# Kernel optimization log

Measured on AMD Instinct MI355X. Metric: run time of the kernel, lower is better.

Reference implementation:

```python
import jax, jax.numpy as jnp
import numpy as np

D_MODEL, D_STATE, D_CONV, EXPAND, HEADDIM, NGROUPS, CHUNK = 1024, 64, 4, 2, 64, 1, 64
D_INNER = EXPAND * D_MODEL          # 2048
NHEADS = D_INNER // HEADDIM         # 32
CONV_DIM = D_INNER + 2 * NGROUPS * D_STATE  # 2176
D_IN_PROJ = 2 * D_INNER + 2 * NGROUPS * D_STATE + NHEADS  # 4256
EPS = 1e-5


def segsum(x):
    """x: (..., T) -> (..., T, T) with out[i,j]=sum_{j<k<=i} x[k], -inf above diag."""
    T = x.shape[-1]
    i = jnp.arange(T)[:, None]
    j = jnp.arange(T)[None, :]
    xr = jnp.where(i > j, x[..., :, None], 0.0)   # keep x[...,i] at (i,j) when i>j
    s = jnp.cumsum(xr, axis=-2)
    return jnp.where(i >= j, s, -jnp.inf)


def setup_inputs() -> dict:
    key = jax.random.key(0)
    ks = jax.random.split(key, 10)
    B, L = 4, 4096
    u = jax.random.normal(ks[0], (B, L, D_MODEL), dtype=jnp.float32)
    in_proj_w = jax.random.normal(ks[1], (D_IN_PROJ, D_MODEL), dtype=jnp.float32) * (D_MODEL ** -0.5)
    conv_w = jax.random.normal(ks[2], (CONV_DIM, D_CONV), dtype=jnp.float32) * (D_CONV ** -0.5)
    conv_b = jax.random.normal(ks[3], (CONV_DIM,), dtype=jnp.float32) * 0.02
    init_states = jax.random.normal(ks[4], (NHEADS, HEADDIM, D_STATE), dtype=jnp.float32) * 0.02
    # dt_bias = inv softplus of dt sampled log-uniform in [1e-3, 1e-1]
    dt = jnp.exp(jax.random.uniform(ks[5], (NHEADS,)) * (np.log(0.1) - np.log(0.001)) + np.log(0.001))
    dt = jnp.clip(dt, 1e-4, None)
    dt_bias = dt + jnp.log(-jnp.expm1(-dt))
    A_log = jnp.log(jax.random.uniform(ks[6], (NHEADS,), minval=1.0, maxval=16.0))
    D = jnp.ones((NHEADS,), dtype=jnp.float32)
    norm_w = jnp.ones((D_INNER,), dtype=jnp.float32)
    out_proj_w = jax.random.normal(ks[7], (D_MODEL, D_INNER), dtype=jnp.float32) * (D_INNER ** -0.5)
    return {"u": u, "in_proj_w": in_proj_w, "conv_w": conv_w, "conv_b": conv_b,
            "init_states": init_states, "dt_bias": dt_bias, "A_log": A_log, "D": D,
            "norm_w": norm_w, "out_proj_w": out_proj_w}


def _forward(u, in_proj_w, conv_w, conv_b, init_states, dt_bias, A_log, D, norm_w, out_proj_w):
    b, L, _ = u.shape
    zxbcdt = jnp.einsum('bld,ed->ble', u, in_proj_w)
    z = zxbcdt[..., :D_INNER]
    xBC = zxbcdt[..., D_INNER:D_INNER + CONV_DIM]
    dt = jax.nn.softplus(zxbcdt[..., D_INNER + CONV_DIM:] + dt_bias)  # (b,L,h)
    # causal depthwise conv1d (padding=K-1, truncated to L) + SiLU
    xp = jnp.pad(xBC, ((0, 0), (D_CONV - 1, 0), (0, 0)))
    xBC = sum(xp[:, k:k + L, :] * conv_w[:, k] for k in range(D_CONV)) + conv_b
    xBC = jax.nn.silu(xBC)
    x = xBC[..., :D_INNER].reshape(b, L, NHEADS, HEADDIM)
    Bm = xBC[..., D_INNER:D_INNER + NGROUPS * D_STATE].reshape(b, L, NGROUPS, D_STATE)
    Cm = xBC[..., D_INNER + NGROUPS * D_STATE:].reshape(b, L, NGROUPS, D_STATE)
    A = -jnp.exp(A_log)  # (h,)
    # broadcast groups to heads (torch einsum broadcasts size-1 group dim)
    Bm = jnp.repeat(Bm, NHEADS // NGROUPS, axis=2)
    Cm = jnp.repeat(Cm, NHEADS // NGROUPS, axis=2)
    X = x * dt[..., None]          # (b,L,h,p)
    Adt = A * dt                   # (b,L,h)
    c = L // CHUNK
    Xc = X.reshape(b, c, CHUNK, NHEADS, HEADDIM)
    Bc = Bm.reshape(b, c, CHUNK, NHEADS, D_STATE)
    Cc = Cm.reshape(b, c, CHUNK, NHEADS, D_STATE)
    Ac = Adt.reshape(b, c, CHUNK, NHEADS).transpose(0, 3, 1, 2)  # (b,h,c,l)
    A_cumsum = jnp.cumsum(Ac, axis=-1)
    Lmat = jnp.exp(segsum(Ac))  # (b,h,c,l,l)
    Y_diag = jnp.einsum('bclhn,bcshn,bhcls,bcshp->bclhp', Cc, Bc, Lmat, Xc)
    decay_states = jnp.exp(A_cumsum[..., -1:] - A_cumsum)  # (b,h,c,l)
    states = jnp.einsum('bclhn,bhcl,bclhp->bchpn', Bc, decay_states, Xc)
    init = jnp.broadcast_to(init_states, (b,) + init_states.shape)[:, None]  # (b,1,h,p,n)
    states = jnp.concatenate([init, states], axis=1)  # (b,c+1,h,p,n)
    decay_chunk = jnp.exp(segsum(jnp.pad(A_cumsum[..., -1], ((0, 0), (0, 0), (1, 0)))))
    new_states = jnp.einsum('bhzc,bchpn->bzhpn', decay_chunk, states)
    states = new_states[:, :-1]
    state_decay_out = jnp.exp(A_cumsum)
    Y_off = jnp.einsum('bclhn,bchpn,bhcl->bclhp', Cc, states, state_decay_out)
    Y = (Y_diag + Y_off).reshape(b, L, NHEADS, HEADDIM) + x * D[:, None]
    y = Y.reshape(b, L, D_INNER)
    # gated RMSNorm (gate before norm)
    y = y * jax.nn.silu(z)
    y = y * jax.lax.rsqrt(jnp.mean(y * y, axis=-1, keepdims=True) + EPS) * norm_w
    return jnp.einsum('bld,ed->ble', y, out_proj_w)


def reference(u, in_proj_w, conv_w, conv_b, init_states, dt_bias, A_log, D, norm_w, out_proj_w):
    return _forward(u, in_proj_w, conv_w, conv_b, init_states, dt_bias, A_log, D, norm_w, out_proj_w)
```

## Files before the change

kernel.cpp:

```cpp
#include <hip/hip_runtime.h>
#include <math.h>

#define BATCH  4
#define LSEQ   4096
#define DMODEL 1024
#define DINNER 2048
#define NH     32
#define HD     64
#define DSTATE 64
#define CONVD  2176
#define NPROJ  4352
#define ZROW   4224
#define NCHUNK 64

typedef __attribute__((ext_vector_type(8))) short bf16x8;
typedef __attribute__((ext_vector_type(4))) float f32x4;

__device__ __forceinline__ float sigm(float x){ return 1.f/(1.f+expf(-x)); }

__device__ __forceinline__ unsigned short f2bf(float x){
    unsigned u = __float_as_uint(x);
    unsigned r = (u + 0x7fffu + ((u>>16)&1u)) >> 16;
    return (unsigned short)r;
}
__device__ __forceinline__ float bf2f(unsigned short h){
    return __uint_as_float(((unsigned)h)<<16);
}

__device__ __forceinline__ void gl2lds16(const unsigned short* g, short* l){
    __builtin_amdgcn_global_load_lds(
        (const __attribute__((address_space(1))) unsigned int*)g,
        (__attribute__((address_space(3))) unsigned int*)l, 16, 0, 0);
}

__global__ __launch_bounds__(256)
void f32_to_bf16(const float* __restrict__ in, unsigned short* __restrict__ o, size_t n)
{
    size_t i = ((size_t)blockIdx.x*256 + threadIdx.x)*8;
    if (i >= n) return;
    float4 a = *(const float4*)(in + i);
    float4 b = *(const float4*)(in + i + 4);
    uint4 v;
    v.x = (unsigned)f2bf(a.x) | ((unsigned)f2bf(a.y)<<16);
    v.y = (unsigned)f2bf(a.z) | ((unsigned)f2bf(a.w)<<16);
    v.z = (unsigned)f2bf(b.x) | ((unsigned)f2bf(b.y)<<16);
    v.w = (unsigned)f2bf(b.z) | ((unsigned)f2bf(b.w)<<16);
    *(uint4*)(o + i) = v;
}

template<int EPI>
__global__ __launch_bounds__(256)
void gemm_mfma(const unsigned short* __restrict__ A,
               const unsigned short* __restrict__ B,
               int K, int lda, int ldc, int ntiles, int Mrows,
               float* __restrict__ Cf,
               unsigned short* __restrict__ zxbc,
               float* __restrict__ dtout,
               const float* __restrict__ dt_bias,
               unsigned short* __restrict__ halo)
{
    __shared__ short As[2][128*64];
    __shared__ short Bs[2][128*64];
    const int tid  = threadIdx.x;
    const int wave = tid >> 6;
    const int lane = tid & 63;

    const int GM  = 16;
    const int pid = blockIdx.x;
    const int gsz = GM * ntiles;
    const int grp = pid / gsz;
    const int rem = pid - grp*gsz;
    const int bm  = (grp*GM + (rem & (GM-1))) * 128;
    const int bn  = (rem / GM) * 128;

    const int wr = (wave >> 1) * 64;
    const int wc = (wave & 1) * 64;
    const int quad = lane >> 4;
    const int l15  = lane & 15;

    f32x4 acc[4][4];
    #pragma unroll
    for (int i=0;i<4;i++)
        #pragma unroll
        for (int j=0;j<4;j++)
            acc[i][j] = (f32x4){0.f,0.f,0.f,0.f};

    const int srow8 = lane >> 3;
    const int scolx = ((lane & 7) ^ srow8) * 8;
    const int rsw   = (l15 & 7);

    const unsigned short* pa = A + (size_t)(bm + srow8)*lda + scolx;
    const unsigned short* pb = B + (size_t)(bn + srow8)*K   + scolx;

    const int nkt = K >> 6;

    #pragma unroll
    for (int s=0; s<4; s++){
        int t = wave*4 + s;
        gl2lds16(pa + (size_t)(t*8)*lda, &As[0][t*512]);
        gl2lds16(pb + (size_t)(t*8)*K,   &Bs[0][t*512]);
    }
    __syncthreads();

    for (int kt = 0; kt < nkt; ++kt){
        if (kt+1 < nkt){
            const int nb_ = (kt+1) & 1;
            const int ko  = (kt+1) << 6;
            #pragma unroll
            for (int s=0; s<4; s++){
                int t = wave*4 + s;
                gl2lds16(pa + (size_t)(t*8)*lda + ko, &As[nb_][t*512]);
                gl2lds16(pb + (size_t)(t*8)*K   + ko, &Bs[nb_][t*512]);
            }
        }
        const short* Asl = &As[kt & 1][0];
        const short* Bsl = &Bs[kt & 1][0];
        #pragma unroll
        for (int ks=0; ks<2; ks++){
            const int co = ((ks*4 + quad) ^ rsw) << 3;
            bf16x8 af[4], bg[4];
            #pragma unroll
            for (int i=0;i<4;i++)
                af[i] = *(const bf16x8*)&Asl[(wr + i*16 + l15)*64 + co];
            #pragma unroll
            for (int j=0;j<4;j++)
                bg[j] = *(const bf16x8*)&Bsl[(wc + j*16 + l15)*64 + co];
            #pragma unroll
            for (int i=0;i<4;i++)
                #pragma unroll
                for (int j=0;j<4;j++)
                    acc[i][j] = __builtin_amdgcn_mfma_f32_16x16x32_bf16(af[i], bg[j], acc[i][j], 0,0,0);
        }
        __syncthreads();
    }

    if (EPI == 0){
        #pragma unroll
        for (int i=0;i<4;i++)
            #pragma unroll
            for (int j=0;j<4;j++){
                int col = bn + wc + j*16 + l15;
                #pragma unroll
                for (int r=0;r<4;r++){
                    int row = bm + wr + i*16 + quad*4 + r;
                    Cf[(size_t)row*ldc + col] = acc[i][j][r];
                }
            }
    } else {
        if (bn < DINNER){
            #pragma unroll
            for (int i=0;i<4;i++)
                #pragma unroll
                for (int r=0;r<4;r++){
                    int row = bm + wr + i*16 + quad*4 + r;
                    #pragma unroll
                    for (int j=0;j<4;j++){
                        int col = bn + wc + j*16 + l15;
                        zxbc[(size_t)row*ZROW + col] = f2bf(acc[i][j][r]);
                    }
                }
        } else if (bn < DINNER + CONVD){
            #pragma unroll
            for (int i=0;i<4;i++)
                #pragma unroll
                for (int r=0;r<4;r++){
                    int row = bm + wr + i*16 + quad*4 + r;
                    int rel = row & 63;
                    int seg = (row >> 6) + 1;
                    #pragma unroll
                    for (int j=0;j<4;j++){
                        int col = bn + wc + j*16 + l15;
                        unsigned short v = f2bf(acc[i][j][r]);
                        zxbc[(size_t)row*ZROW + col] = v;
                        if (rel >= 61 && seg*64 < Mrows)
                            halo[((size_t)(seg*3 + (rel-61)))*CONVD + (col - DINNER)] = v;
                    }
                }
        } else if (wc == 0){
            #pragma unroll
            for (int j=0;j<2;j++){
                int h = j*16 + l15;
                #pragma unroll
                for (int i=0;i<4;i++)
                    #pragma unroll
                    for (int r=0;r<4;r++){
                        int row = bm + wr + i*16 + quad*4 + r;
                        float t = acc[i][j][r] + dt_bias[h];
                        dtout[(size_t)row*NH + h] = (t > 20.f) ? t : log1pf(expf(t));
                    }
            }
        }
    }
}

__global__ __launch_bounds__(256)
void conv_inplace(unsigned short* __restrict__ zxbc,
                  const unsigned short* __restrict__ halo,
                  const float* __restrict__ conv_w, const float* __restrict__ conv_b)
{
    int c = blockIdx.x*256 + threadIdx.x;
    if (c >= CONVD) return;
    int seg = blockIdx.y;
    const float w0=conv_w[c*4+0], w1=conv_w[c*4+1], w2=conv_w[c*4+2], w3=conv_w[c*4+3];
    const float bias = conv_b[c];
    float x0=0.f, x1=0.f, x2=0.f;
    if ((seg & 63) != 0){
        const unsigned short* hp = halo + (size_t)(seg*3)*CONVD + c;
        x0 = bf2f(hp[0]); x1 = bf2f(hp[CONVD]); x2 = bf2f(hp[2*CONVD]);
    }
    unsigned short* p = zxbc + (size_t)(seg*64)*ZROW + DINNER + c;
    for (int i=0;i<64;i++){
        float x3 = bf2f(*p);
        float v = fmaf(w0,x0,fmaf(w1,x1,fmaf(w2,x2,fmaf(w3,x3,bias))));
        *p = f2bf(v * sigm(v));
        x0=x1; x1=x2; x2=x3; p += ZROW;
    }
}

__global__ __launch_bounds__(256)
void states_intra(const unsigned short* __restrict__ zxbc,
                  const float* __restrict__ dtbuf,
                  const float* __restrict__ A_log,
                  unsigned short* __restrict__ locst,
                  float* __restrict__ acsbuf,
                  float* __restrict__ csumbuf)
{
    const int h = blockIdx.x, c = blockIdx.y;
    __shared__ unsigned short XT[64*72];
    __shared__ unsigned short BT[64*72];
    __shared__ float dt_sh[64], acs_sh[64], w_sh[64];
    const int tid = threadIdx.x;
    const size_t row0 = (size_t)(c*64)*ZROW;

    if (tid < 64) dt_sh[tid] = dtbuf[(size_t)(c*64+tid)*NH + h];
    __syncthreads();
    if (tid == 0){
        float Ah = -expf(A_log[h]); float s = 0.f;
        for (int l=0;l<64;l++){ s = fmaf(Ah, dt_sh[l], s); acs_sh[l] = s; }
    }
    __syncthreads();
    const float a63 = acs_sh[63];
    if (tid < 64){
        float a = acs_sh[tid];
        acsbuf[((size_t)c*NH + h)*64 + tid] = a;
        w_sh[tid] = expf(a63 - a) * dt_sh[tid];
    }
    if (tid == 0) csumbuf[(size_t)c*NH + h] = a63;
    __syncthreads();

    {
        const int l  = tid >> 2;
        const int f4 = tid & 3;
        const unsigned short* xr = zxbc + row0 + (size_t)l*ZROW;
        const float w = w_sh[l];
        #pragma unroll
        for (int q=0;q<4;q++){
            int col = f4*4 + q*16;
            uint2 xv = *(const uint2*)(xr + DINNER + h*HD + col);
            uint2 bv = *(const uint2*)(xr + DINNER + DINNER + col);
            XT[(col+0)*72 + l] = (unsigned short)(xv.x & 0xffff);
            XT[(col+1)*72 + l] = (unsigned short)(xv.x >> 16);
            XT[(col+2)*72 + l] = (unsigned short)(xv.y & 0xffff);
            XT[(col+3)*72 + l] = (unsigned short)(xv.y >> 16);
            BT[(col+0)*72 + l] = f2bf(bf2f((unsigned short)(bv.x & 0xffff))*w);
            BT[(col+1)*72 + l] = f2bf(bf2f((unsigned short)(bv.x >> 16))*w);
            BT[(col+2)*72 + l] = f2bf(bf2f((unsigned short)(bv.y & 0xffff))*w);
            BT[(col+3)*72 + l] = f2bf(bf2f((unsigned short)(bv.y >> 16))*w);
        }
    }
    __syncthreads();

    const int wave = tid >> 6, lane = tid & 63;
    const int quad = lane >> 4, l15 = lane & 15;
    f32x4 acc[4];
    #pragma unroll
    for (int j=0;j<4;j++) acc[j] = (f32x4){0.f,0.f,0.f,0.f};
    #pragma unroll
    for (int ks=0;ks<2;ks++){
        bf16x8 af = *(const bf16x8*)&XT[(wave*16 + l15)*72 + ks*32 + quad*8];
        #pragma unroll
        for (int j=0;j<4;j++){
            bf16x8 bf = *(const bf16x8*)&BT[(j*16 + l15)*72 + ks*32 + quad*8];
            acc[j] = __builtin_amdgcn_mfma_f32_16x16x32_bf16(af, bf, acc[j], 0,0,0);
        }
    }
    const size_t sbase = ((size_t)c*NH + h)*4096;
    #pragma unroll
    for (int j=0;j<4;j++)
        #pragma unroll
        for (int r=0;r<4;r++){
            int p = wave*16 + quad*4 + r;
            int n = j*16 + l15;
            locst[sbase + (size_t)p*64 + n] = f2bf(acc[j][r]);
        }
}

__global__ __launch_bounds__(256)
void chunk_scan(unsigned short* __restrict__ states,
                const float* __restrict__ csumbuf,
                const float* __restrict__ init_states)
{
    const int h = blockIdx.x, half = blockIdx.y, b = blockIdx.z;
    __shared__ float cs_sh[64];
    const int tid = threadIdx.x;
    if (tid < 64) cs_sh[tid] = csumbuf[(size_t)(b*64 + tid)*NH + h];
    __syncthreads();
    const int e0 = half*2048 + tid*8;
    float S[8];
    {
        const float4* ip = (const float4*)(init_states + (size_t)h*4096 + e0);
        float4 v0 = ip[0], v1 = ip[1];
        S[0]=v0.x; S[1]=v0.y; S[2]=v0.z; S[3]=v0.w;
        S[4]=v1.x; S[5]=v1.y; S[6]=v1.z; S[7]=v1.w;
    }
    for (int zg=0; zg<8; zg++){
        uint4 L[8];
        #pragma unroll
        for (int k=0;k<8;k++)
            L[k] = *(const uint4*)(states + ((size_t)(b*64 + zg*8+k)*NH + h)*4096 + e0);
        #pragma unroll
        for (int k=0;k<8;k++){
            int z = zg*8 + k;
            float dec = expf(cs_sh[z]);
            uint4 o;
            o.x = (unsigned)f2bf(S[0]) | ((unsigned)f2bf(S[1])<<16);
            o.y = (unsigned)f2bf(S[2]) | ((unsigned)f2bf(S[3])<<16);
            o.z = (unsigned)f2bf(S[4]) | ((unsigned)f2bf(S[5])<<16);
            o.w = (unsigned)f2bf(S[6]) | ((unsigned)f2bf(S[7])<<16);
            *(uint4*)(states + ((size_t)(b*64 + z)*NH + h)*4096 + e0) = o;
            unsigned a[4] = {L[k].x, L[k].y, L[k].z, L[k].w};
            #pragma unroll
            for (int q=0;q<4;q++){
                float lo = bf2f((unsigned short)(a[q]&0xffff));
                float hi = bf2f((unsigned short)(a[q]>>16));
                S[q*2+0] = fmaf(dec, S[q*2+0], lo);
                S[q*2+1] = fmaf(dec, S[q*2+1], hi);
            }
        }
    }
}

__global__ __launch_bounds__(256)
void y_fused(unsigned short* __restrict__ zxbc,
             const float* __restrict__ dtbuf,
             const unsigned short* __restrict__ entst,
             const float* __restrict__ acsbuf,
             const float* __restrict__ Dvec)
{
    const int h = blockIdx.x, c = blockIdx.y;
    __shared__ unsigned short Cr[64*72];
    __shared__ unsigned short Ce[64*72];
    __shared__ unsigned short Bm[64*72];
    __shared__ unsigned short XT[64*72];
    __shared__ unsigned short Sv[64*72];
    __shared__ float acs_sh[64], dt_sh[64], ea_sh[64];
    const int tid = threadIdx.x;
    const size_t row0 = (size_t)(c*64)*ZROW;
    const size_t sbase = ((size_t)c*NH + h)*4096;

    if (tid < 64){
        float a = acsbuf[((size_t)c*NH + h)*64 + tid];
        acs_sh[tid] = a;
        ea_sh[tid]  = expf(a);
        dt_sh[tid]  = dtbuf[(size_t)(c*64 + tid)*NH + h];
    }
    __syncthreads();

    {
        const int l  = tid >> 2;
        const int f4 = tid & 3;
        const unsigned short* xr = zxbc + row0 + (size_t)l*ZROW;
        const float el = ea_sh[l];
        #pragma unroll
        for (int q=0;q<4;q++){
            int col = f4*4 + q*16;
            uint2 cv = *(const uint2*)(xr + DINNER + DINNER + DSTATE + col);
            uint2 bv = *(const uint2*)(xr + DINNER + DINNER + col);
            uint2 xv = *(const uint2*)(xr + DINNER + h*HD + col);
            *(uint2*)&Cr[l*72 + col] = cv;
            *(uint2*)&Bm[l*72 + col] = bv;
            unsigned short* ce = &Ce[l*72 + col];
            ce[0] = f2bf(bf2f((unsigned short)(cv.x & 0xffff))*el);
            ce[1] = f2bf(bf2f((unsigned short)(cv.x >> 16))*el);
            ce[2] = f2bf(bf2f((unsigned short)(cv.y & 0xffff))*el);
            ce[3] = f2bf(bf2f((unsigned short)(cv.y >> 16))*el);
            XT[(col+0)*72 + l] = (unsigned short)(xv.x & 0xffff);
            XT[(col+1)*72 + l] = (unsigned short)(xv.x >> 16);
            XT[(col+2)*72 + l] = (unsigned short)(xv.y & 0xffff);
            XT[(col+3)*72 + l] = (unsigned short)(xv.y >> 16);
            *(uint2*)&Sv[l*72 + col] = *(const uint2*)(entst + sbase + (size_t)l*64 + col);
        }
    }
    __syncthreads();

    const int wave = tid >> 6, lane = tid & 63;
    const int quad = lane >> 4, l15 = lane & 15;

    f32x4 g[4];
    #pragma unroll
    for (int j=0;j<4;j++) g[j] = (f32x4){0.f,0.f,0.f,0.f};
    #pragma unroll
    for (int ks=0;ks<2;ks++){
        bf16x8 af = *(const bf16x8*)&Cr[(wave*16 + l15)*72 + ks*32 + quad*8];
        #pragma unroll
        for (int j=0;j<4;j++){
            bf16x8 bf = *(const bf16x8*)&Bm[(j*16 + l15)*72 + ks*32 + quad*8];
            g[j] = __builtin_amdgcn_mfma_f32_16x16x32_bf16(af, bf, g[j], 0,0,0);
        }
    }
    __syncthreads();

    const float Dh = Dvec[h];
    #pragma unroll
    for (int j=0;j<4;j++)
        #pragma unroll
        for (int r=0;r<4;r++){
            int l = wave*16 + quad*4 + r;
            int s = j*16 + l15;
            float v = (s <= l) ? g[j][r]*expf(acs_sh[l]-acs_sh[s])*dt_sh[s] : 0.f;
            if (s == l) v += Dh;
            Bm[l*72 + s] = f2bf(v);
        }
    __syncthreads();

    f32x4 y[4];
    #pragma unroll
    for (int j=0;j<4;j++) y[j] = (f32x4){0.f,0.f,0.f,0.f};
    #pragma unroll
    for (int ks=0;ks<2;ks++){
        bf16x8 a1 = *(const bf16x8*)&Bm[(wave*16 + l15)*72 + ks*32 + quad*8];
        bf16x8 a2 = *(const bf16x8*)&Ce[(wave*16 + l15)*72 + ks*32 + quad*8];
        #pragma unroll
        for (int j=0;j<4;j++){
            bf16x8 b1 = *(const bf16x8*)&XT[(j*16 + l15)*72 + ks*32 + quad*8];
            bf16x8 b2 = *(const bf16x8*)&Sv[(j*16 + l15)*72 + ks*32 + quad*8];
            y[j] = __builtin_amdgcn_mfma_f32_16x16x32_bf16(a1, b1, y[j], 0,0,0);
            y[j] = __builtin_amdgcn_mfma_f32_16x16x32_bf16(a2, b2, y[j], 0,0,0);
        }
    }

    #pragma unroll
    for (int j=0;j<4;j++)
        #pragma unroll
        for (int r=0;r<4;r++){
            int l = wave*16 + quad*4 + r;
            int p = j*16 + l15;
            zxbc[row0 + (size_t)l*ZROW + DINNER + h*HD + p] = f2bf(y[j][r]);
        }
}

__global__ __launch_bounds__(256)
void gate_norm(unsigned short* __restrict__ zxbc, const float* __restrict__ norm_w)
{
    const int m = blockIdx.x;
    const int tid = threadIdx.x;
    unsigned short* row = zxbc + (size_t)m*ZROW;
    uint4 zv = *(const uint4*)(row + tid*8);
    uint4 yv = *(const uint4*)(row + DINNER + tid*8);
    unsigned zz[4] = {zv.x, zv.y, zv.z, zv.w};
    unsigned yy[4] = {yv.x, yv.y, yv.z, yv.w};
    float g[8];
    float acc = 0.f;
    #pragma unroll
    for (int q=0;q<4;q++){
        float zl = bf2f((unsigned short)(zz[q]&0xffff));
        float zh = bf2f((unsigned short)(zz[q]>>16));
        float yl = bf2f((unsigned short)(yy[q]&0xffff));
        float yh = bf2f((unsigned short)(yy[q]>>16));
        g[q*2+0] = yl * zl * sigm(zl);
        g[q*2+1] = yh * zh * sigm(zh);
        acc += g[q*2]*g[q*2] + g[q*2+1]*g[q*2+1];
    }
    #pragma unroll
    for (int o=32;o>0;o>>=1) acc += __shfl_down(acc, o, 64);
    __shared__ float red[4];
    if ((tid & 63)==0) red[tid>>6] = acc;
    __syncthreads();
    float tot = red[0]+red[1]+red[2]+red[3];
    float scale = rsqrtf(tot * (1.f/2048.f) + 1e-5f);
    const float* nw = norm_w + tid*8;
    float4 w0 = *(const float4*)nw;
    float4 w1 = *(const float4*)(nw+4);
    float Wv[8] = {w0.x,w0.y,w0.z,w0.w,w1.x,w1.y,w1.z,w1.w};
    uint4 ov;
    unsigned ow[4];
    #pragma unroll
    for (int q=0;q<4;q++){
        unsigned short lo = f2bf(g[q*2+0]*scale*Wv[q*2+0]);
        unsigned short hi = f2bf(g[q*2+1]*scale*Wv[q*2+1]);
        ow[q] = (unsigned)lo | ((unsigned)hi<<16);
    }
    ov.x=ow[0]; ov.y=ow[1]; ov.z=ow[2]; ov.w=ow[3];
    *(uint4*)(row + tid*8) = ov;
}

extern "C" void kernel_launch(void* const* d_in, const int* in_sizes, int n_in,
                              void* d_out, int out_size, void* d_ws, size_t ws_size,
                              hipStream_t stream) {
    const float* u           = (const float*)d_in[0];
    const float* in_proj_w   = (const float*)d_in[1];
    const float* conv_w      = (const float*)d_in[2];
    const float* conv_b      = (const float*)d_in[3];
    const float* init_states = (const float*)d_in[4];
    const float* dt_bias     = (const float*)d_in[5];
    const float* A_log       = (const float*)d_in[6];
    const float* Dv          = (const float*)d_in[7];
    const float* norm_w      = (const float*)d_in[8];
    const float* out_proj_w  = (const float*)d_in[9];
    float* out = (float*)d_out;
    char* wsb = (char*)d_ws;

    const size_t BIG_BYTES = 226197504;
    const bool big = (ws_size >= BIG_BYTES);
    const int nb = big ? BATCH : 1;
    const size_t Mrows = (size_t)nb * LSEQ;

    size_t off = 0;
    unsigned short* zxbc    = (unsigned short*)(wsb + off); off += Mrows*ZROW*2;
    unsigned short* statesz = (unsigned short*)(wsb + off);
    unsigned short* ubf     = statesz;
    off += Mrows/64 * NH*HD*DSTATE*2;
    unsigned short* wibf    = (unsigned short*)(wsb + off); off += (size_t)NPROJ*DMODEL*2;
    unsigned short* woutbf  = (unsigned short*)(wsb + off); off += (size_t)DMODEL*DINNER*2;
    float*          dtbuf   = (float*)(wsb + off);   off += Mrows*NH*4;
    float*          acsbuf  = (float*)(wsb + off);   off += Mrows/64 * NH*64*4;
    float*          csumbuf = (float*)(wsb + off);   off += Mrows/64 * NH*4;
    unsigned short* halo    = (unsigned short*)(wsb + off); off += Mrows/64 * 3*CONVD*2;

    f32_to_bf16<<<dim3((4256*1024/8 + 255)/256), 256, 0, stream>>>(
        in_proj_w, wibf, (size_t)4256*1024);
    f32_to_bf16<<<dim3(1024*2048/8/256), 256, 0, stream>>>(
        out_proj_w, woutbf, (size_t)1024*2048);

    const int npass = big ? 1 : BATCH;
    for (int b=0; b<npass; b++){
        const float* ub   = u   + (size_t)b*LSEQ*DMODEL;
        float*       outb = out + (size_t)b*LSEQ*DMODEL;
        const int mt = (int)(Mrows/128);

        f32_to_bf16<<<dim3(Mrows*DMODEL/8/256), 256, 0, stream>>>(
            ub, ubf, Mrows*DMODEL);
        gemm_mfma<1><<<dim3((NPROJ/128) * mt), 256, 0, stream>>>(
            ubf, wibf, DMODEL, DMODEL, 0, NPROJ/128, (int)Mrows,
            nullptr, zxbc, dtbuf, dt_bias, halo);
        conv_inplace<<<dim3(9, (unsigned)(Mrows/64)), 256, 0, stream>>>(
            zxbc, halo, conv_w, conv_b);
        states_intra<<<dim3(NH, (unsigned)(Mrows/64)), 256, 0, stream>>>(
            zxbc, dtbuf, A_log, statesz, acsbuf, csumbuf);
        chunk_scan<<<dim3(NH, 2, nb), 256, 0, stream>>>(
            statesz, csumbuf, init_states);
        y_fused<<<dim3(NH, (unsigned)(Mrows/64)), 256, 0, stream>>>(
            zxbc, dtbuf, statesz, acsbuf, Dv);
        gate_norm<<<dim3((unsigned)Mrows), 256, 0, stream>>>(zxbc, norm_w);
        gemm_mfma<0><<<dim3((DMODEL/128) * mt), 256, 0, stream>>>(
            zxbc, woutbf, DINNER, ZROW, DMODEL, DMODEL/128, (int)Mrows,
            outb, nullptr, nullptr, nullptr, nullptr);
    }
}
```

Baseline: 584.9 us.

## Process four heads per block to reuse B/C tiles and CB product

states_intra and y_fused now each handle four heads per block. The shared B tile and the C·Bᵀ Gram matrix are loaded and computed once per chunk and reused across heads, where before they were recomputed for every head. states_intra swaps the serial single-thread cumsum for a wave-level shuffle scan and moves the decay weight from B onto X. y_fused drops the exp(A)-scaled C copy and applies that scaling in fp32 when combining the two accumulators. This cuts redundant global loads and MFMA work, but leaves a quarter as many blocks and serialises the per-head loop inside each block.

```diff
diff --git a/kernel.cpp b/kernel.cpp
--- a/kernel.cpp
+++ b/kernel.cpp
@@ -225,74 +225,87 @@
                   float* __restrict__ acsbuf,
                   float* __restrict__ csumbuf)
 {
-    const int h = blockIdx.x, c = blockIdx.y;
-    __shared__ unsigned short XT[64*72];
+    const int hg = blockIdx.x, c = blockIdx.y;
     __shared__ unsigned short BT[64*72];
-    __shared__ float dt_sh[64], acs_sh[64], w_sh[64];
-    const int tid = threadIdx.x;
+    __shared__ unsigned short XTw[64*72];
+    __shared__ float w_sh4[4][64];
+    const int tid  = threadIdx.x;
+    const int wave = tid >> 6, lane = tid & 63;
     const size_t row0 = (size_t)(c*64)*ZROW;
-
-    if (tid < 64) dt_sh[tid] = dtbuf[(size_t)(c*64+tid)*NH + h];
-    __syncthreads();
-    if (tid == 0){
-        float Ah = -expf(A_log[h]); float s = 0.f;
-        for (int l=0;l<64;l++){ s = fmaf(Ah, dt_sh[l], s); acs_sh[l] = s; }
-    }
-    __syncthreads();
-    const float a63 = acs_sh[63];
-    if (tid < 64){
-        float a = acs_sh[tid];
-        acsbuf[((size_t)c*NH + h)*64 + tid] = a;
-        w_sh[tid] = expf(a63 - a) * dt_sh[tid];
-    }
-    if (tid == 0) csumbuf[(size_t)c*NH + h] = a63;
-    __syncthreads();
 
     {
         const int l  = tid >> 2;
         const int f4 = tid & 3;
-        const unsigned short* xr = zxbc + row0 + (size_t)l*ZROW;
-        const float w = w_sh[l];
+        const unsigned short* xr = zxbc + row0 + (size_t)l*ZROW + DINNER + DINNER;
         #pragma unroll
         for (int q=0;q<4;q++){
             int col = f4*4 + q*16;
-            uint2 xv = *(const uint2*)(xr + DINNER + h*HD + col);
-            uint2 bv = *(const uint2*)(xr + DINNER + DINNER + col);
-            XT[(col+0)*72 + l] = (unsigned short)(xv.x & 0xffff);
-            XT[(col+1)*72 + l] = (unsigned short)(xv.x >> 16);
-            XT[(col+2)*72 + l] = (unsigned short)(xv.y & 0xffff);
-            XT[(col+3)*72 + l] = (unsigned short)(xv.y >> 16);
-            BT[(col+0)*72 + l] = f2bf(bf2f((unsigned short)(bv.x & 0xffff))*w);
-            BT[(col+1)*72 + l] = f2bf(bf2f((unsigned short)(bv.x >> 16))*w);
-            BT[(col+2)*72 + l] = f2bf(bf2f((unsigned short)(bv.y & 0xffff))*w);
-            BT[(col+3)*72 + l] = f2bf(bf2f((unsigned short)(bv.y >> 16))*w);
-        }
+            uint2 bv = *(const uint2*)(xr + col);
+            BT[(col+0)*72 + l] = (unsigned short)(bv.x & 0xffff);
+            BT[(col+1)*72 + l] = (unsigned short)(bv.x >> 16);
+            BT[(col+2)*72 + l] = (unsigned short)(bv.y & 0xffff);
+            BT[(col+3)*72 + l] = (unsigned short)(bv.y >> 16);
+        }
+    }
+    {
+        const int h = hg*4 + wave;
+        float dt = dtbuf[(size_t)(c*64 + lane)*NH + h];
+        float Ah = -expf(A_log[h]);
+        float s  = Ah * dt;
+        #pragma unroll
+        for (int o=1; o<64; o<<=1){
+            float t = __shfl_up(s, o, 64);
+            if (lane >= o) s += t;
+        }
+        float a63 = __shfl(s, 63, 64);
+        acsbuf[((size_t)c*NH + h)*64 + lane] = s;
+        w_sh4[wave][lane] = expf(a63 - s) * dt;
+        if (lane == 0) csumbuf[(size_t)c*NH + h] = a63;
     }
     __syncthreads();
 
-    const int wave = tid >> 6, lane = tid & 63;
     const int quad = lane >> 4, l15 = lane & 15;
-    f32x4 acc[4];
-    #pragma unroll
-    for (int j=0;j<4;j++) acc[j] = (f32x4){0.f,0.f,0.f,0.f};
-    #pragma unroll
-    for (int ks=0;ks<2;ks++){
-        bf16x8 af = *(const bf16x8*)&XT[(wave*16 + l15)*72 + ks*32 + quad*8];
-        #pragma unroll
-        for (int j=0;j<4;j++){
-            bf16x8 bf = *(const bf16x8*)&BT[(j*16 + l15)*72 + ks*32 + quad*8];
-            acc[j] = __builtin_amdgcn_mfma_f32_16x16x32_bf16(af, bf, acc[j], 0,0,0);
-        }
-    }
-    const size_t sbase = ((size_t)c*NH + h)*4096;
-    #pragma unroll
-    for (int j=0;j<4;j++)
-        #pragma unroll
-        for (int r=0;r<4;r++){
-            int p = wave*16 + quad*4 + r;
-            int n = j*16 + l15;
-            locst[sbase + (size_t)p*64 + n] = f2bf(acc[j][r]);
-        }
+    for (int hh=0; hh<4; hh++){
+        const int h = hg*4 + hh;
+        if (hh) __syncthreads();
+        {
+            const int l  = tid >> 2;
+            const int f4 = tid & 3;
+            const unsigned short* xr = zxbc + row0 + (size_t)l*ZROW + DINNER + h*HD;
+            const float w = w_sh4[hh][l];
+            #pragma unroll
+            for (int q=0;q<4;q++){
+                int col = f4*4 + q*16;
+                uint2 xv = *(const uint2*)(xr + col);
+                XTw[(col+0)*72 + l] = f2bf(bf2f((unsigned short)(xv.x & 0xffff))*w);
+                XTw[(col+1)*72 + l] = f2bf(bf2f((unsigned short)(xv.x >> 16))*w);
+                XTw[(col+2)*72 + l] = f2bf(bf2f((unsigned short)(xv.y & 0xffff))*w);
+                XTw[(col+3)*72 + l] = f2bf(bf2f((unsigned short)(xv.y >> 16))*w);
+            }
+        }
+        __syncthreads();
+        f32x4 acc[4];
+        #pragma unroll
+        for (int j=0;j<4;j++) acc[j] = (f32x4){0.f,0.f,0.f,0.f};
+        #pragma unroll
+        for (int ks=0;ks<2;ks++){
+            bf16x8 af = *(const bf16x8*)&XTw[(wave*16 + l15)*72 + ks*32 + quad*8];
+            #pragma unroll
+            for (int j=0;j<4;j++){
+                bf16x8 bf = *(const bf16x8*)&BT[(j*16 + l15)*72 + ks*32 + quad*8];
+                acc[j] = __builtin_amdgcn_mfma_f32_16x16x32_bf16(af, bf, acc[j], 0,0,0);
+            }
+        }
+        const size_t sbase = ((size_t)c*NH + h)*4096;
+        #pragma unroll
+        for (int j=0;j<4;j++)
+            #pragma unroll
+            for (int r=0;r<4;r++){
+                int p = wave*16 + quad*4 + r;
+                int n = j*16 + l15;
+                locst[sbase + (size_t)p*64 + n] = f2bf(acc[j][r]);
+            }
+    }
 }
 
 __global__ __launch_bounds__(256)
@@ -347,48 +360,24 @@
              const float* __restrict__ acsbuf,
              const float* __restrict__ Dvec)
 {
-    const int h = blockIdx.x, c = blockIdx.y;
+    const int hg = blockIdx.x, c = blockIdx.y;
     __shared__ unsigned short Cr[64*72];
-    __shared__ unsigned short Ce[64*72];
-    __shared__ unsigned short Bm[64*72];
+    __shared__ unsigned short Bs[64*72];
     __shared__ unsigned short XT[64*72];
     __shared__ unsigned short Sv[64*72];
     __shared__ float acs_sh[64], dt_sh[64], ea_sh[64];
     const int tid = threadIdx.x;
     const size_t row0 = (size_t)(c*64)*ZROW;
-    const size_t sbase = ((size_t)c*NH + h)*4096;
-
-    if (tid < 64){
-        float a = acsbuf[((size_t)c*NH + h)*64 + tid];
-        acs_sh[tid] = a;
-        ea_sh[tid]  = expf(a);
-        dt_sh[tid]  = dtbuf[(size_t)(c*64 + tid)*NH + h];
-    }
-    __syncthreads();
 
     {
         const int l  = tid >> 2;
         const int f4 = tid & 3;
         const unsigned short* xr = zxbc + row0 + (size_t)l*ZROW;
-        const float el = ea_sh[l];
         #pragma unroll
         for (int q=0;q<4;q++){
             int col = f4*4 + q*16;
-            uint2 cv = *(const uint2*)(xr + DINNER + DINNER + DSTATE + col);
-            uint2 bv = *(const uint2*)(xr + DINNER + DINNER + col);
-            uint2 xv = *(const uint2*)(xr + DINNER + h*HD + col);
-            *(uint2*)&Cr[l*72 + col] = cv;
-            *(uint2*)&Bm[l*72 + col] = bv;
-            unsigned short* ce = &Ce[l*72 + col];
-            ce[0] = f2bf(bf2f((unsigned short)(cv.x & 0xffff))*el);
-            ce[1] = f2bf(bf2f((unsigned short)(cv.x >> 16))*el);
-            ce[2] = f2bf(bf2f((unsigned short)(cv.y & 0xffff))*el);
-            ce[3] = f2bf(bf2f((unsigned short)(cv.y >> 16))*el);
-            XT[(col+0)*72 + l] = (unsigned short)(xv.x & 0xffff);
-            XT[(col+1)*72 + l] = (unsigned short)(xv.x >> 16);
-            XT[(col+2)*72 + l] = (unsigned short)(xv.y & 0xffff);
-            XT[(col+3)*72 + l] = (unsigned short)(xv.y >> 16);
-            *(uint2*)&Sv[l*72 + col] = *(const uint2*)(entst + sbase + (size_t)l*64 + col);
+            *(uint2*)&Cr[l*72 + col] = *(const uint2*)(xr + DINNER + DINNER + DSTATE + col);
+            *(uint2*)&Bs[l*72 + col] = *(const uint2*)(xr + DINNER + DINNER + col);
         }
     }
     __syncthreads();
@@ -404,49 +393,76 @@
         bf16x8 af = *(const bf16x8*)&Cr[(wave*16 + l15)*72 + ks*32 + quad*8];
         #pragma unroll
         for (int j=0;j<4;j++){
-            bf16x8 bf = *(const bf16x8*)&Bm[(j*16 + l15)*72 + ks*32 + quad*8];
+            bf16x8 bf = *(const bf16x8*)&Bs[(j*16 + l15)*72 + ks*32 + quad*8];
             g[j] = __builtin_amdgcn_mfma_f32_16x16x32_bf16(af, bf, g[j], 0,0,0);
         }
     }
-    __syncthreads();
-
-    const float Dh = Dvec[h];
-    #pragma unroll
-    for (int j=0;j<4;j++)
-        #pragma unroll
-        for (int r=0;r<4;r++){
-            int l = wave*16 + quad*4 + r;
-            int s = j*16 + l15;
-            float v = (s <= l) ? g[j][r]*expf(acs_sh[l]-acs_sh[s])*dt_sh[s] : 0.f;
-            if (s == l) v += Dh;
-            Bm[l*72 + s] = f2bf(v);
-        }
-    __syncthreads();
-
-    f32x4 y[4];
-    #pragma unroll
-    for (int j=0;j<4;j++) y[j] = (f32x4){0.f,0.f,0.f,0.f};
-    #pragma unroll
-    for (int ks=0;ks<2;ks++){
-        bf16x8 a1 = *(const bf16x8*)&Bm[(wave*16 + l15)*72 + ks*32 + quad*8];
-        bf16x8 a2 = *(const bf16x8*)&Ce[(wave*16 + l15)*72 + ks*32 + quad*8];
-        #pragma unroll
-        for (int j=0;j<4;j++){
-            bf16x8 b1 = *(const bf16x8*)&XT[(j*16 + l15)*72 + ks*32 + quad*8];
-            bf16x8 b2 = *(const bf16x8*)&Sv[(j*16 + l15)*72 + ks*32 + quad*8];
-            y[j] = __builtin_amdgcn_mfma_f32_16x16x32_bf16(a1, b1, y[j], 0,0,0);
-            y[j] = __builtin_amdgcn_mfma_f32_16x16x32_bf16(a2, b2, y[j], 0,0,0);
-        }
-    }
-
-    #pragma unroll
-    for (int j=0;j<4;j++)
-        #pragma unroll
-        for (int r=0;r<4;r++){
-            int l = wave*16 + quad*4 + r;
-            int p = j*16 + l15;
-            zxbc[row0 + (size_t)l*ZROW + DINNER + h*HD + p] = f2bf(y[j][r]);
-        }
+
+    for (int hh=0; hh<4; hh++){
+        const int h = hg*4 + hh;
+        __syncthreads();
+        if (tid < 64){
+            float a = acsbuf[((size_t)c*NH + h)*64 + tid];
+            acs_sh[tid] = a;
+            ea_sh[tid]  = expf(a);
+            dt_sh[tid]  = dtbuf[(size_t)(c*64 + tid)*NH + h];
+        }
+        {
+            const int l  = tid >> 2;
+            const int f4 = tid & 3;
+            const unsigned short* xr = zxbc + row0 + (size_t)l*ZROW;
+            const size_t sbase = ((size_t)c*NH + h)*4096;
+            #pragma unroll
+            for (int q=0;q<4;q++){
+                int col = f4*4 + q*16;
+                uint2 xv = *(const uint2*)(xr + DINNER + h*HD + col);
+                XT[(col+0)*72 + l] = (unsigned short)(xv.x & 0xffff);
+                XT[(col+1)*72 + l] = (unsigned short)(xv.x >> 16);
+                XT[(col+2)*72 + l] = (unsigned short)(xv.y & 0xffff);
+                XT[(col+3)*72 + l] = (unsigned short)(xv.y >> 16);
+                *(uint2*)&Sv[l*72 + col] = *(const uint2*)(entst + sbase + (size_t)l*64 + col);
+            }
+        }
+        __syncthreads();
+
+        const float Dh = Dvec[h];
+        #pragma unroll
+        for (int j=0;j<4;j++)
+            #pragma unroll
+            for (int r=0;r<4;r++){
+                int l = wave*16 + quad*4 + r;
+                int s = j*16 + l15;
+                float v = (s <= l) ? g[j][r]*expf(acs_sh[l]-acs_sh[s])*dt_sh[s] : 0.f;
+                if (s == l) v += Dh;
+                Bs[l*72 + s] = f2bf(v);
+            }
+        __syncthreads();
+
+        f32x4 y1[4], y2[4];
+        #pragma unroll
+        for (int j=0;j<4;j++){ y1[j] = (f32x4){0.f,0.f,0.f,0.f}; y2[j] = (f32x4){0.f,0.f,0.f,0.f}; }
+        #pragma unroll
+        for (int ks=0;ks<2;ks++){
+            bf16x8 a1 = *(const bf16x8*)&Bs[(wave*16 + l15)*72 + ks*32 + quad*8];
+            bf16x8 a2 = *(const bf16x8*)&Cr[(wave*16 + l15)*72 + ks*32 + quad*8];
+            #pragma unroll
+            for (int j=0;j<4;j++){
+                bf16x8 b1 = *(const bf16x8*)&XT[(j*16 + l15)*72 + ks*32 + quad*8];
+                bf16x8 b2 = *(const bf16x8*)&Sv[(j*16 + l15)*72 + ks*32 + quad*8];
+                y1[j] = __builtin_amdgcn_mfma_f32_16x16x32_bf16(a1, b1, y1[j], 0,0,0);
+                y2[j] = __builtin_amdgcn_mfma_f32_16x16x32_bf16(a2, b2, y2[j], 0,0,0);
+            }
+        }
+        #pragma unroll
+        for (int j=0;j<4;j++)
+            #pragma unroll
+            for (int r=0;r<4;r++){
+                int l = wave*16 + quad*4 + r;
+                int p = j*16 + l15;
+                zxbc[row0 + (size_t)l*ZROW + DINNER + h*HD + p] =
+                    f2bf(y1[j][r] + ea_sh[l]*y2[j][r]);
+            }
+    }
 }
 
 __global__ __launch_bounds__(256)
@@ -545,11 +561,11 @@
             nullptr, zxbc, dtbuf, dt_bias, halo);
         conv_inplace<<<dim3(9, (unsigned)(Mrows/64)), 256, 0, stream>>>(
             zxbc, halo, conv_w, conv_b);
-        states_intra<<<dim3(NH, (unsigned)(Mrows/64)), 256, 0, stream>>>(
+        states_intra<<<dim3(NH/4, (unsigned)(Mrows/64)), 256, 0, stream>>>(
             zxbc, dtbuf, A_log, statesz, acsbuf, csumbuf);
         chunk_scan<<<dim3(NH, 2, nb), 256, 0, stream>>>(
             statesz, csumbuf, init_states);
-        y_fused<<<dim3(NH, (unsigned)(Mrows/64)), 256, 0, stream>>>(
+        y_fused<<<dim3(NH/4, (unsigned)(Mrows/64)), 256, 0, stream>>>(
             zxbc, dtbuf, statesz, acsbuf, Dv);
         gate_norm<<<dim3((unsigned)Mrows), 256, 0, stream>>>(zxbc, norm_w);
         gemm_mfma<0><<<dim3((DMODEL/128) * mt), 256, 0, stream>>>(
```

Result: no change. 576.5 us (-1.4%).
